# Kernel tuning notes

Measured on AMD Instinct MI355X. Metric: run time of the kernel, lower is better.

Reference implementation:

```python
import jax, jax.numpy as jnp
import numpy as np

NUM_EMBEDDINGS = 512
EMBEDDING_DIM = 128
COMMITMENT_COST = 0.25


def setup_inputs() -> dict:
    key = jax.random.key(0)
    k1, k2 = jax.random.split(key)
    inputs = jax.random.normal(k1, (8, EMBEDDING_DIM, 32, 32, 32), dtype=jnp.float32)
    limit = 1.0 / NUM_EMBEDDINGS
    weight = jax.random.uniform(k2, (NUM_EMBEDDINGS, EMBEDDING_DIM), dtype=jnp.float32,
                                minval=-limit, maxval=limit)
    return {"inputs": inputs, "weight": weight}


def reference(inputs, weight):
    sg = jax.lax.stop_gradient
    # (B, C, D, H, W) -> (B, D, H, W, C)
    x = jnp.transpose(inputs, (0, 2, 3, 4, 1))
    C = x.shape[-1]
    flat = x.reshape(-1, C)  # [N, C]
    distances = (jnp.sum(flat * flat, axis=1, keepdims=True)
                 + jnp.sum(weight * weight, axis=1)
                 - 2.0 * flat @ weight.T)
    encoding_indices = jnp.argmin(distances, axis=1)  # [N]
    encodings = jax.nn.one_hot(encoding_indices, weight.shape[0], dtype=jnp.float32)  # [N, E]
    # gather is mathematically identical to encodings @ weight
    quantized = weight[encoding_indices].reshape(x.shape)
    e_latent_loss = jnp.mean((sg(quantized) - x) ** 2)
    q_latent_loss = jnp.mean((quantized - sg(x)) ** 2)
    loss = q_latent_loss + COMMITMENT_COST * e_latent_loss
    # straight-through estimator
    quantized_st = x + sg(quantized - x)
    avg_probs = jnp.mean(encodings, axis=0)
    perplexity = jnp.exp(-jnp.sum(avg_probs * jnp.log(avg_probs + 1e-10)))
    out_q = jnp.transpose(quantized_st, (0, 4, 1, 2, 3))  # back to (B, C, D, H, W)
    return loss, out_q, perplexity, encodings
```

## Files before the change

kernel.cpp:

```cpp
#include <hip/hip_runtime.h>
#include <math.h>

#define CDIM 128
#define EDIM 512
#define BLK 256
#define MT 64
#define NVEC 262144
#define SPATIAL 32768
#define QELEMS 33554432LL
#define TIE_T 4e-6f

typedef __bf16 bf16x8 __attribute__((ext_vector_type(8)));
typedef float  f32x4  __attribute__((ext_vector_type(4)));

struct WS {
  float  wnh[EDIM];
  int    counts[EDIM];
  double lossAcc;
  double _pad;
  unsigned short wph[EDIM * CDIM];
  unsigned short wpl[EDIM * CDIM];
};

__device__ inline unsigned short bfbits(float f) {
  union { __bf16 b; unsigned short u; } cv; cv.b = (__bf16)f; return cv.u;
}
__device__ inline void split2(float x0, float x1, unsigned& hv, unsigned& lv) {
  unsigned short h0 = bfbits(x0), h1 = bfbits(x1);
  float r0 = x0 - __uint_as_float((unsigned)h0 << 16);
  float r1 = x1 - __uint_as_float((unsigned)h1 << 16);
  unsigned short l0 = bfbits(r0), l1 = bfbits(r1);
  hv = (unsigned)h0 | ((unsigned)h1 << 16);
  lv = (unsigned)l0 | ((unsigned)l1 << 16);
}

__device__ inline void ins3(float v, int ix, float& m1, float& m2, float& m3,
                            int& j1, int& j2) {
  bool q1 = (v < m1) || (v == m1 && ix < j1);
  bool q2 = (v < m2) || (v == m2 && ix < j2);
  if (q1)      { m3 = m2; m2 = m1; j2 = j1; m1 = v; j1 = ix; }
  else if (q2) { m3 = m2; m2 = v; j2 = ix; }
  else if (v < m3) { m3 = v; }
}

__global__ __launch_bounds__(256) void vq_pre(const float* __restrict__ wt,
                                              WS* __restrict__ ws, int buildWP) {
  const int tid = threadIdx.x, bid = blockIdx.x;
  const int e = bid * 8 + (tid >> 5);
  const int k0 = (tid & 31) * 4;
  float4 F = *(const float4*)(wt + (size_t)e * CDIM + k0);
  float nrm = F.x * F.x + F.y * F.y + F.z * F.z + F.w * F.w;
#pragma unroll
  for (int off = 1; off < 32; off <<= 1) nrm += __shfl_xor(nrm, off);
  if ((tid & 31) == 0) ws->wnh[e] = 0.5f * nrm;
  if (tid < 8) ws->counts[bid * 8 + tid] = 0;
  if (bid == 0 && tid == 0) ws->lossAcc = 0.0;
  if (buildWP) {
    const int etile = e >> 4, row = e & 15;
    const int kt = k0 >> 5, g = (k0 >> 3) & 3, j0 = k0 & 7;
    size_t idx = ((size_t)(etile * 4 + kt) * 64 + g * 16 + row) * 8 + j0;
    unsigned hv0, lv0, hv1, lv1;
    split2(F.x, F.y, hv0, lv0);
    split2(F.z, F.w, hv1, lv1);
    *(uint2*)&ws->wph[idx] = make_uint2(hv0, hv1);
    *(uint2*)&ws->wpl[idx] = make_uint2(lv0, lv1);
  }
}

__device__ double score64(const float* __restrict__ in, const float* __restrict__ wt,
                          size_t xoff, int e) {
  const float* w = wt + (size_t)e * CDIM;
  double a = 0.0;
  for (int c = 0; c < CDIM; ++c) {
    double wd = (double)w[c];
    double xv = (double)in[xoff + (size_t)c * SPATIAL];
    a = fma(wd, fma(0.5, wd, -xv), a);
  }
  return a;
}

template <bool USEWP>
__global__ __launch_bounds__(BLK, 4) void vq_main(const float* __restrict__ in,
                                                  const float* __restrict__ wt,
                                                  WS* __restrict__ ws,
                                                  float* __restrict__ out_q,
                                                  float* __restrict__ enc) {
  __shared__ __align__(16) unsigned short xhi[8192];
  __shared__ __align__(16) unsigned short xlo[8192];
  __shared__ float cb1[MT][5], cb2[MT][5], cb3[MT][5];
  __shared__ int   ci1[MT][5], ci2[MT][5];
  __shared__ int    sIdx[MT];
  __shared__ double lredw[4];

  const int tid = threadIdx.x;
  const int n0 = blockIdx.x * MT;
  const int b  = n0 >> 15;
  const int s0 = n0 & (SPATIAL - 1);
  const size_t ibase = (size_t)b * CDIM * SPATIAL;

  {
    const int mq = tid & 15;
    const int cg = tid >> 4;
    const int m0 = mq * 4, c0 = cg * 8;
    float4 F[8];
#pragma unroll
    for (int i = 0; i < 8; ++i)
      F[i] = *(const float4*)(in + ibase + (size_t)(c0 + i) * SPATIAL + s0 + m0);
#pragma unroll
    for (int mi = 0; mi < 4; ++mi) {
      const int m = m0 + mi;
      unsigned hv[4], lv[4];
#pragma unroll
      for (int p = 0; p < 4; ++p)
        split2(((const float*)&F[2 * p])[mi], ((const float*)&F[2 * p + 1])[mi],
               hv[p], lv[p]);
      const int fm = (m & 15) ^ ((m & 15) >> 2);
      const int elem = cg * 512 + (m >> 4) * 128 + fm * 8;
      *(uint4*)&xhi[elem] = make_uint4(hv[0], hv[1], hv[2], hv[3]);
      *(uint4*)&xlo[elem] = make_uint4(lv[0], lv[1], lv[2], lv[3]);
    }
  }
  __syncthreads();

  const int lane = tid & 63, wv = tid >> 6;
  const int col = lane & 15, g = lane >> 4;
  const int fcol = col ^ (col >> 2);

  float b1[4], b2[4], b3[4]; int i1[4], i2[4];
#pragma unroll
  for (int i = 0; i < 4; ++i) { b1[i] = 1e30f; b2[i] = 1e30f; b3[i] = 1e30f; i1[i] = 0; i2[i] = 0; }

  for (int ch = 0; ch < 8; ++ch) {
    const int etile = ch * 4 + wv;
    bf16x8 ah[4], al[4];
    if (USEWP) {
#pragma unroll
      for (int kt = 0; kt < 4; ++kt) {
        size_t aoff = ((size_t)(etile * 4 + kt) * 64 + lane) * 8;
        ah[kt] = *(const bf16x8*)&ws->wph[aoff];
        al[kt] = *(const bf16x8*)&ws->wpl[aoff];
      }
    } else {
      const int e = etile * 16 + col;
#pragma unroll
      for (int kt = 0; kt < 4; ++kt) {
        const float* wp = wt + (size_t)e * CDIM + kt * 32 + g * 8;
        float4 Fa = *(const float4*)wp, Fb = *(const float4*)(wp + 4);
        float xf[8] = {Fa.x, Fa.y, Fa.z, Fa.w, Fb.x, Fb.y, Fb.z, Fb.w};
        bf16x8 h, l;
#pragma unroll
        for (int j = 0; j < 8; ++j) {
          __bf16 hb = (__bf16)xf[j];
          float r = xf[j] - (float)hb;
          h[j] = hb; l[j] = (__bf16)r;
        }
        ah[kt] = h; al[kt] = l;
      }
    }

    f32x4 acc[4];
#pragma unroll
    for (int mt = 0; mt < 4; ++mt) {
      f32x4 a = {0.f, 0.f, 0.f, 0.f};
#pragma unroll
      for (int kt = 0; kt < 4; ++kt) {
        const int xb = (kt * 4 + g) * 512 + mt * 128 + fcol * 8;
        bf16x8 bh = *(const bf16x8*)&xhi[xb];
        bf16x8 bl = *(const bf16x8*)&xlo[xb];
        a = __builtin_amdgcn_mfma_f32_16x16x32_bf16(ah[kt], bh, a, 0, 0, 0);
        a = __builtin_amdgcn_mfma_f32_16x16x32_bf16(ah[kt], bl, a, 0, 0, 0);
        a = __builtin_amdgcn_mfma_f32_16x16x32_bf16(al[kt], bh, a, 0, 0, 0);
      }
      acc[mt] = a;
    }

    const int e0 = ch * 64 + wv * 16 + g * 4;
    const float4 wn = *(const float4*)&ws->wnh[e0];
#pragma unroll
    for (int mt = 0; mt < 4; ++mt) {
#pragma unroll
      for (int r = 0; r < 4; ++r) {
        float sc = ((const float*)&wn)[r] - acc[mt][r];
        ins3(sc, e0 + r, b1[mt], b2[mt], b3[mt], i1[mt], i2[mt]);
      }
    }
  }

#pragma unroll
  for (int mt = 0; mt < 4; ++mt) {
#pragma unroll
    for (int sh = 0; sh < 2; ++sh) {
      const int off = 16 << sh;
      float p1 = __shfl_xor(b1[mt], off), p2 = __shfl_xor(b2[mt], off),
            p3 = __shfl_xor(b3[mt], off);
      int q1 = __shfl_xor(i1[mt], off), q2 = __shfl_xor(i2[mt], off);
      ins3(p1, q1, b1[mt], b2[mt], b3[mt], i1[mt], i2[mt]);
      ins3(p2, q2, b1[mt], b2[mt], b3[mt], i1[mt], i2[mt]);
      ins3(p3, 0x7fffffff, b1[mt], b2[mt], b3[mt], i1[mt], i2[mt]);
    }
  }
  if (g == 0) {
#pragma unroll
    for (int mt = 0; mt < 4; ++mt) {
      const int m = mt * 16 + col;
      cb1[m][wv] = b1[mt]; cb2[m][wv] = b2[mt]; cb3[m][wv] = b3[mt];
      ci1[m][wv] = i1[mt]; ci2[m][wv] = i2[mt];
    }
  }
  __syncthreads();

  if (tid < MT) {
    const int vec = tid;
    float m1 = cb1[vec][0], m2 = cb2[vec][0], m3 = cb3[vec][0];
    int j1 = ci1[vec][0], j2 = ci2[vec][0];
#pragma unroll
    for (int t = 1; t < 4; ++t) {
      ins3(cb1[vec][t], ci1[vec][t], m1, m2, m3, j1, j2);
      ins3(cb2[vec][t], ci2[vec][t], m1, m2, m3, j1, j2);
      ins3(cb3[vec][t], 0x7fffffff, m1, m2, m3, j1, j2);
    }
    int bi = j1;
    const size_t xoff = ibase + s0 + vec;
    if (m3 - m1 < TIE_T) {
      double bd = 1e300; int bj = 0;
      for (int e = 0; e < EDIM; ++e) {
        double a = score64(in, wt, xoff, e);
        if (a < bd) { bd = a; bj = e; }
      }
      bi = bj;
    } else if (m2 - m1 < TIE_T) {
      double s1 = score64(in, wt, xoff, j1);
      double s2 = score64(in, wt, xoff, j2);
      if (s2 < s1 || (s2 == s1 && j2 < j1)) bi = j2;
    }
    sIdx[vec] = bi;
    atomicAdd(&ws->counts[bi], 1);
  }
  __syncthreads();

  {
    const int vec = tid & (MT - 1);
    const int qd  = tid >> 6;
    const int bi  = sIdx[vec];
    const float* wq = wt + (size_t)bi * CDIM;
    const size_t gbase = ibase + s0 + vec;
    const int fv = (vec & 15) ^ ((vec & 15) >> 2);
    double ls = 0.0;
#pragma unroll
    for (int cc = 0; cc < 32; cc += 4) {
      const int c = qd * 32 + cc;
      const int elem = (c >> 3) * 512 + (vec >> 4) * 128 + fv * 8 + (c & 7);
      uint2 hq = *(const uint2*)&xhi[elem];
      uint2 lq = *(const uint2*)&xlo[elem];
      float xs0 = __uint_as_float(hq.x << 16)        + __uint_as_float(lq.x << 16);
      float xs1 = __uint_as_float(hq.x & 0xffff0000u) + __uint_as_float(lq.x & 0xffff0000u);
      float xs2 = __uint_as_float(hq.y << 16)        + __uint_as_float(lq.y << 16);
      float xs3 = __uint_as_float(hq.y & 0xffff0000u) + __uint_as_float(lq.y & 0xffff0000u);
      float4 qv = *(const float4*)(wq + c);
      __builtin_nontemporal_store(qv.x, out_q + gbase + (size_t)(c + 0) * SPATIAL);
      __builtin_nontemporal_store(qv.y, out_q + gbase + (size_t)(c + 1) * SPATIAL);
      __builtin_nontemporal_store(qv.z, out_q + gbase + (size_t)(c + 2) * SPATIAL);
      __builtin_nontemporal_store(qv.w, out_q + gbase + (size_t)(c + 3) * SPATIAL);
      double d0 = (double)qv.x - (double)xs0; ls = fma(d0, d0, ls);
      double d1 = (double)qv.y - (double)xs1; ls = fma(d1, d1, ls);
      double d2 = (double)qv.z - (double)xs2; ls = fma(d2, d2, ls);
      double d3 = (double)qv.w - (double)xs3; ls = fma(d3, d3, ls);
    }
#pragma unroll
    for (int off = 32; off > 0; off >>= 1) ls += __shfl_down(ls, off);
    if (lane == 0) lredw[wv] = ls;
  }
  __syncthreads();
  if (tid == 0) atomicAdd(&ws->lossAcc, lredw[0] + lredw[1] + lredw[2] + lredw[3]);

  {
    const size_t r0 = (size_t)blockIdx.x * MT;
    const int c0 = tid * 2;
    unsigned long long* e2 = (unsigned long long*)enc;
    for (int r = 0; r < MT; ++r) {
      int idx = sIdx[r];
      union { float2 f; unsigned long long u; } cvt;
      cvt.f.x = (idx == c0) ? 1.0f : 0.0f;
      cvt.f.y = (idx == c0 + 1) ? 1.0f : 0.0f;
      __builtin_nontemporal_store(cvt.u, e2 + (r0 + (size_t)r) * (EDIM / 2) + tid);
    }
  }
}

__global__ __launch_bounds__(512) void vq_fin(const WS* __restrict__ ws, float* __restrict__ out) {
  __shared__ double red[EDIM];
  int t = threadIdx.x;
  double p = (double)ws->counts[t] * (1.0 / (double)NVEC);
  red[t] = p * log(p + 1e-10);
  __syncthreads();
  for (int off = 256; off > 0; off >>= 1) {
    if (t < off) red[t] += red[t + off];
    __syncthreads();
  }
  if (t == 0) {
    out[0] = (float)(1.25 * ws->lossAcc / (double)QELEMS);
    out[1 + QELEMS] = (float)exp(-red[0]);
  }
}

extern "C" void kernel_launch(void* const* d_in, const int* in_sizes, int n_in,
                              void* d_out, int out_size, void* d_ws, size_t ws_size,
                              hipStream_t stream) {
  const float* in = (const float*)d_in[0];
  const float* wt = (const float*)d_in[1];
  float* out = (float*)d_out;
  WS* ws = (WS*)d_ws;

  float* out_q = out + 1;
  float* enc   = out + 2 + QELEMS;

  const bool useWP = (ws_size >= sizeof(WS));
  vq_pre<<<dim3(64), dim3(256), 0, stream>>>(wt, ws, useWP ? 1 : 0);
  if (useWP)
    vq_main<true><<<dim3(NVEC / MT), dim3(BLK), 0, stream>>>(in, wt, ws, out_q, enc);
  else
    vq_main<false><<<dim3(NVEC / MT), dim3(BLK), 0, stream>>>(in, wt, ws, out_q, enc);
  vq_fin<<<dim3(1), dim3(512), 0, stream>>>(ws, out);
}
```

Before: 1.275 ms.

## Stage codebook chunks through LDS with register double-buffering and block-local histogram

```diff
diff --git a/kernel.cpp b/kernel.cpp
--- a/kernel.cpp
+++ b/kernel.cpp
@@ -5,6 +5,9 @@
 #define EDIM 512
 #define BLK 256
 #define MT 64
+#define ECH 64
+#define NCH (EDIM / ECH)
+#define WROW 136
 #define NVEC 262144
 #define SPATIAL 32768
 #define QELEMS 33554432LL
@@ -56,14 +59,11 @@
   if (tid < 8) ws->counts[bid * 8 + tid] = 0;
   if (bid == 0 && tid == 0) ws->lossAcc = 0.0;
   if (buildWP) {
-    const int etile = e >> 4, row = e & 15;
-    const int kt = k0 >> 5, g = (k0 >> 3) & 3, j0 = k0 & 7;
-    size_t idx = ((size_t)(etile * 4 + kt) * 64 + g * 16 + row) * 8 + j0;
     unsigned hv0, lv0, hv1, lv1;
     split2(F.x, F.y, hv0, lv0);
     split2(F.z, F.w, hv1, lv1);
-    *(uint2*)&ws->wph[idx] = make_uint2(hv0, hv1);
-    *(uint2*)&ws->wpl[idx] = make_uint2(lv0, lv1);
+    *(uint2*)&ws->wph[(size_t)e * CDIM + k0] = make_uint2(hv0, hv1);
+    *(uint2*)&ws->wpl[(size_t)e * CDIM + k0] = make_uint2(lv0, lv1);
   }
 }
 
@@ -80,15 +80,15 @@
 }
 
 template <bool USEWP>
-__global__ __launch_bounds__(BLK, 4) void vq_main(const float* __restrict__ in,
+__global__ __launch_bounds__(BLK, 2) void vq_main(const float* __restrict__ in,
                                                   const float* __restrict__ wt,
                                                   WS* __restrict__ ws,
                                                   float* __restrict__ out_q,
                                                   float* __restrict__ enc) {
   __shared__ __align__(16) unsigned short xhi[8192];
   __shared__ __align__(16) unsigned short xlo[8192];
-  __shared__ float cb1[MT][5], cb2[MT][5], cb3[MT][5];
-  __shared__ int   ci1[MT][5], ci2[MT][5];
+  __shared__ __align__(16) unsigned short wls[2 * ECH * WROW];
+  __shared__ int    hist[EDIM];
   __shared__ int    sIdx[MT];
   __shared__ double lredw[4];
 
@@ -97,6 +97,8 @@
   const int b  = n0 >> 15;
   const int s0 = n0 & (SPATIAL - 1);
   const size_t ibase = (size_t)b * CDIM * SPATIAL;
+
+  for (int e = tid; e < EDIM; e += BLK) hist[e] = 0;
 
   {
     const int mq = tid & 15;
@@ -120,42 +122,64 @@
       *(uint4*)&xlo[elem] = make_uint4(lv[0], lv[1], lv[2], lv[3]);
     }
   }
-  __syncthreads();
 
   const int lane = tid & 63, wv = tid >> 6;
   const int col = lane & 15, g = lane >> 4;
   const int fcol = col ^ (col >> 2);
 
+  const int se  = tid >> 2;
+  const int skq = (tid & 3) * 32;
+
   float b1[4], b2[4], b3[4]; int i1[4], i2[4];
 #pragma unroll
   for (int i = 0; i < 4; ++i) { b1[i] = 1e30f; b2[i] = 1e30f; b3[i] = 1e30f; i1[i] = 0; i2[i] = 0; }
 
-  for (int ch = 0; ch < 8; ++ch) {
-    const int etile = ch * 4 + wv;
+  uint4 Gh[4], Gl[4], Hh[4], Hl[4];
+#pragma unroll
+  for (int i = 0; i < 4; ++i) {
+    Hh[i] = make_uint4(0, 0, 0, 0);
+    Hl[i] = make_uint4(0, 0, 0, 0);
+  }
+
+  auto loadW = [&](int ch, uint4* Th, uint4* Tl) {
+    if (USEWP) {
+      const uint4* ph = (const uint4*)&ws->wph[(size_t)(ch * ECH + se) * CDIM + skq];
+      const uint4* pl = (const uint4*)&ws->wpl[(size_t)(ch * ECH + se) * CDIM + skq];
+#pragma unroll
+      for (int i = 0; i < 4; ++i) { Th[i] = ph[i]; Tl[i] = pl[i]; }
+    } else {
+      const float* wp = wt + (size_t)(ch * ECH + se) * CDIM + skq;
+#pragma unroll
+      for (int i = 0; i < 4; ++i) {
+        float4 A = *(const float4*)(wp + i * 8);
+        float4 B = *(const float4*)(wp + i * 8 + 4);
+        unsigned hv0, lv0, hv1, lv1, hv2, lv2, hv3, lv3;
+        split2(A.x, A.y, hv0, lv0); split2(A.z, A.w, hv1, lv1);
+        split2(B.x, B.y, hv2, lv2); split2(B.z, B.w, hv3, lv3);
+        Th[i] = make_uint4(hv0, hv1, hv2, hv3);
+        Tl[i] = make_uint4(lv0, lv1, lv2, lv3);
+      }
+    }
+  };
+
+  loadW(0, Gh, Gl);
+
+  for (int ch = 0; ch < NCH; ++ch) {
+    __syncthreads();
+#pragma unroll
+    for (int i = 0; i < 4; ++i) {
+      *(uint4*)&wls[se * WROW + skq + i * 8] = Gh[i];
+      *(uint4*)&wls[ECH * WROW + se * WROW + skq + i * 8] = Gl[i];
+    }
+    if (ch + 1 < NCH) loadW(ch + 1, Hh, Hl);
+    __syncthreads();
+
     bf16x8 ah[4], al[4];
-    if (USEWP) {
-#pragma unroll
-      for (int kt = 0; kt < 4; ++kt) {
-        size_t aoff = ((size_t)(etile * 4 + kt) * 64 + lane) * 8;
-        ah[kt] = *(const bf16x8*)&ws->wph[aoff];
-        al[kt] = *(const bf16x8*)&ws->wpl[aoff];
-      }
-    } else {
-      const int e = etile * 16 + col;
-#pragma unroll
-      for (int kt = 0; kt < 4; ++kt) {
-        const float* wp = wt + (size_t)e * CDIM + kt * 32 + g * 8;
-        float4 Fa = *(const float4*)wp, Fb = *(const float4*)(wp + 4);
-        float xf[8] = {Fa.x, Fa.y, Fa.z, Fa.w, Fb.x, Fb.y, Fb.z, Fb.w};
-        bf16x8 h, l;
-#pragma unroll
-        for (int j = 0; j < 8; ++j) {
-          __bf16 hb = (__bf16)xf[j];
-          float r = xf[j] - (float)hb;
-          h[j] = hb; l[j] = (__bf16)r;
-        }
-        ah[kt] = h; al[kt] = l;
-      }
+#pragma unroll
+    for (int kt = 0; kt < 4; ++kt) {
+      const int rb = (wv * 16 + col) * WROW + kt * 32 + g * 8;
+      ah[kt] = *(const bf16x8*)&wls[rb];
+      al[kt] = *(const bf16x8*)&wls[ECH * WROW + rb];
     }
 
     f32x4 acc[4];
@@ -174,7 +198,7 @@
       acc[mt] = a;
     }
 
-    const int e0 = ch * 64 + wv * 16 + g * 4;
+    const int e0 = ch * ECH + wv * 16 + g * 4;
     const float4 wn = *(const float4*)&ws->wnh[e0];
 #pragma unroll
     for (int mt = 0; mt < 4; ++mt) {
@@ -184,6 +208,8 @@
         ins3(sc, e0 + r, b1[mt], b2[mt], b3[mt], i1[mt], i2[mt]);
       }
     }
+#pragma unroll
+    for (int i = 0; i < 4; ++i) { Gh[i] = Hh[i]; Gl[i] = Hl[i]; }
   }
 
 #pragma unroll
@@ -199,42 +225,53 @@
       ins3(p3, 0x7fffffff, b1[mt], b2[mt], b3[mt], i1[mt], i2[mt]);
     }
   }
-  if (g == 0) {
-#pragma unroll
-    for (int mt = 0; mt < 4; ++mt) {
-      const int m = mt * 16 + col;
-      cb1[m][wv] = b1[mt]; cb2[m][wv] = b2[mt]; cb3[m][wv] = b3[mt];
-      ci1[m][wv] = i1[mt]; ci2[m][wv] = i2[mt];
-    }
-  }
+
   __syncthreads();
-
-  if (tid < MT) {
-    const int vec = tid;
-    float m1 = cb1[vec][0], m2 = cb2[vec][0], m3 = cb3[vec][0];
-    int j1 = ci1[vec][0], j2 = ci2[vec][0];
-#pragma unroll
-    for (int t = 1; t < 4; ++t) {
-      ins3(cb1[vec][t], ci1[vec][t], m1, m2, m3, j1, j2);
-      ins3(cb2[vec][t], ci2[vec][t], m1, m2, m3, j1, j2);
-      ins3(cb3[vec][t], 0x7fffffff, m1, m2, m3, j1, j2);
-    }
-    int bi = j1;
-    const size_t xoff = ibase + s0 + vec;
-    if (m3 - m1 < TIE_T) {
-      double bd = 1e300; int bj = 0;
-      for (int e = 0; e < EDIM; ++e) {
-        double a = score64(in, wt, xoff, e);
-        if (a < bd) { bd = a; bj = e; }
-      }
-      bi = bj;
-    } else if (m2 - m1 < TIE_T) {
-      double s1 = score64(in, wt, xoff, j1);
-      double s2 = score64(in, wt, xoff, j2);
-      if (s2 < s1 || (s2 == s1 && j2 < j1)) bi = j2;
-    }
-    sIdx[vec] = bi;
-    atomicAdd(&ws->counts[bi], 1);
+  {
+    char* mb = (char*)wls;
+    float (*cb1)[5] = (float(*)[5])mb;
+    float (*cb2)[5] = (float(*)[5])(mb + 1280);
+    float (*cb3)[5] = (float(*)[5])(mb + 2560);
+    int   (*ci1)[5] = (int(*)[5])(mb + 3840);
+    int   (*ci2)[5] = (int(*)[5])(mb + 5120);
+
+    if (g == 0) {
+#pragma unroll
+      for (int mt = 0; mt < 4; ++mt) {
+        const int m = mt * 16 + col;
+        cb1[m][wv] = b1[mt]; cb2[m][wv] = b2[mt]; cb3[m][wv] = b3[mt];
+        ci1[m][wv] = i1[mt]; ci2[m][wv] = i2[mt];
+      }
+    }
+    __syncthreads();
+
+    if (tid < MT) {
+      const int vec = tid;
+      float m1 = cb1[vec][0], m2 = cb2[vec][0], m3 = cb3[vec][0];
+      int j1 = ci1[vec][0], j2 = ci2[vec][0];
+#pragma unroll
+      for (int t = 1; t < 4; ++t) {
+        ins3(cb1[vec][t], ci1[vec][t], m1, m2, m3, j1, j2);
+        ins3(cb2[vec][t], ci2[vec][t], m1, m2, m3, j1, j2);
+        ins3(cb3[vec][t], 0x7fffffff, m1, m2, m3, j1, j2);
+      }
+      int bi = j1;
+      const size_t xoff = ibase + s0 + vec;
+      if (m3 - m1 < TIE_T) {
+        double bd = 1e300; int bj = 0;
+        for (int e = 0; e < EDIM; ++e) {
+          double a = score64(in, wt, xoff, e);
+          if (a < bd) { bd = a; bj = e; }
+        }
+        bi = bj;
+      } else if (m2 - m1 < TIE_T) {
+        double s1 = score64(in, wt, xoff, j1);
+        double s2 = score64(in, wt, xoff, j2);
+        if (s2 < s1 || (s2 == s1 && j2 < j1)) bi = j2;
+      }
+      sIdx[vec] = bi;
+      atomicAdd(&hist[bi], 1);
+    }
   }
   __syncthreads();
 
@@ -285,6 +322,11 @@
       __builtin_nontemporal_store(cvt.u, e2 + (r0 + (size_t)r) * (EDIM / 2) + tid);
     }
   }
+
+  for (int e = tid; e < EDIM; e += BLK) {
+    int v = hist[e];
+    if (v) atomicAdd(&ws->counts[e], v);
+  }
 }
 
 __global__ __launch_bounds__(512) void vq_fin(const WS* __restrict__ ws, float* __restrict__ out) {
```

Result: faster. 1.058 ms (-17.1%).

## Switch to fp16 split-x MFMA with LDS-staged codebook and wave-level tie resolution

Applied to the files above, without the earlier changes.

```diff
diff --git a/kernel.cpp b/kernel.cpp
--- a/kernel.cpp
+++ b/kernel.cpp
@@ -5,13 +5,15 @@
 #define EDIM 512
 #define BLK 256
 #define MT 64
+#define ECH 64
+#define NCH 8
 #define NVEC 262144
 #define SPATIAL 32768
 #define QELEMS 33554432LL
-#define TIE_T 4e-6f
-
-typedef __bf16 bf16x8 __attribute__((ext_vector_type(8)));
-typedef float  f32x4  __attribute__((ext_vector_type(4)));
+#define TIE_T 2.5e-4f
+
+typedef _Float16 f16x8 __attribute__((ext_vector_type(8)));
+typedef float    f32x4 __attribute__((ext_vector_type(4)));
 
 struct WS {
   float  wnh[EDIM];
@@ -19,20 +21,7 @@
   double lossAcc;
   double _pad;
   unsigned short wph[EDIM * CDIM];
-  unsigned short wpl[EDIM * CDIM];
 };
-
-__device__ inline unsigned short bfbits(float f) {
-  union { __bf16 b; unsigned short u; } cv; cv.b = (__bf16)f; return cv.u;
-}
-__device__ inline void split2(float x0, float x1, unsigned& hv, unsigned& lv) {
-  unsigned short h0 = bfbits(x0), h1 = bfbits(x1);
-  float r0 = x0 - __uint_as_float((unsigned)h0 << 16);
-  float r1 = x1 - __uint_as_float((unsigned)h1 << 16);
-  unsigned short l0 = bfbits(r0), l1 = bfbits(r1);
-  hv = (unsigned)h0 | ((unsigned)h1 << 16);
-  lv = (unsigned)l0 | ((unsigned)l1 << 16);
-}
 
 __device__ inline void ins3(float v, int ix, float& m1, float& m2, float& m3,
                             int& j1, int& j2) {
@@ -56,27 +45,14 @@
   if (tid < 8) ws->counts[bid * 8 + tid] = 0;
   if (bid == 0 && tid == 0) ws->lossAcc = 0.0;
   if (buildWP) {
-    const int etile = e >> 4, row = e & 15;
-    const int kt = k0 >> 5, g = (k0 >> 3) & 3, j0 = k0 & 7;
-    size_t idx = ((size_t)(etile * 4 + kt) * 64 + g * 16 + row) * 8 + j0;
-    unsigned hv0, lv0, hv1, lv1;
-    split2(F.x, F.y, hv0, lv0);
-    split2(F.z, F.w, hv1, lv1);
-    *(uint2*)&ws->wph[idx] = make_uint2(hv0, hv1);
-    *(uint2*)&ws->wpl[idx] = make_uint2(lv0, lv1);
-  }
-}
-
-__device__ double score64(const float* __restrict__ in, const float* __restrict__ wt,
-                          size_t xoff, int e) {
-  const float* w = wt + (size_t)e * CDIM;
-  double a = 0.0;
-  for (int c = 0; c < CDIM; ++c) {
-    double wd = (double)w[c];
-    double xv = (double)in[xoff + (size_t)c * SPATIAL];
-    a = fma(wd, fma(0.5, wd, -xv), a);
-  }
-  return a;
+    union { _Float16 h[4]; uint2 u; } P;
+    P.h[0] = (_Float16)F.x; P.h[1] = (_Float16)F.y;
+    P.h[2] = (_Float16)F.z; P.h[3] = (_Float16)F.w;
+    size_t idx = (size_t)(e >> 6) * 8192 +
+                 (size_t)(((((e >> 4) & 3) * 4 + (k0 >> 5)) * 64) +
+                          ((k0 >> 3) & 3) * 16 + (e & 15)) * 8 + (k0 & 7);
+    *(uint2*)&ws->wph[idx] = P.u;
+  }
 }
 
 template <bool USEWP>
@@ -85,190 +61,214 @@
                                                   WS* __restrict__ ws,
                                                   float* __restrict__ out_q,
                                                   float* __restrict__ enc) {
-  __shared__ __align__(16) unsigned short xhi[8192];
-  __shared__ __align__(16) unsigned short xlo[8192];
-  __shared__ float cb1[MT][5], cb2[MT][5], cb3[MT][5];
-  __shared__ int   ci1[MT][5], ci2[MT][5];
+  __shared__ __align__(16) char uni[32768];
+  __shared__ int    hist[EDIM];
   __shared__ int    sIdx[MT];
   __shared__ double lredw[4];
 
   const int tid = threadIdx.x;
+  const int lane = tid & 63, wv = tid >> 6;
+  const int col = lane & 15, g = lane >> 4;
+  const int fcol = col ^ (col >> 2);
   const int n0 = blockIdx.x * MT;
   const int b  = n0 >> 15;
   const int s0 = n0 & (SPATIAL - 1);
   const size_t ibase = (size_t)b * CDIM * SPATIAL;
 
-  {
-    const int mq = tid & 15;
-    const int cg = tid >> 4;
+  for (int e = tid; e < EDIM; e += BLK) hist[e] = 0;
+
+  uint4 G[4];
+  auto loadG = [&](int ch) {
+    if (USEWP) {
+      const uint4* p = (const uint4*)ws->wph + (size_t)ch * 1024;
+#pragma unroll
+      for (int i = 0; i < 4; ++i) G[i] = p[i * BLK + tid];
+    } else {
+#pragma unroll
+      for (int i = 0; i < 4; ++i) {
+        int q = i * BLK + tid;
+        int e = ch * 64 + (q >> 8) * 16 + (q & 15);
+        int kb = ((q >> 6) & 3) * 32 + ((q >> 4) & 3) * 8;
+        float4 A = *(const float4*)(wt + (size_t)e * CDIM + kb);
+        float4 Bv = *(const float4*)(wt + (size_t)e * CDIM + kb + 4);
+        union { _Float16 h[8]; uint4 u; } P;
+        P.h[0]=(_Float16)A.x; P.h[1]=(_Float16)A.y; P.h[2]=(_Float16)A.z; P.h[3]=(_Float16)A.w;
+        P.h[4]=(_Float16)Bv.x; P.h[5]=(_Float16)Bv.y; P.h[6]=(_Float16)Bv.z; P.h[7]=(_Float16)Bv.w;
+        G[i] = P.u;
+      }
+    }
+  };
+
+  {
+    const int mq = tid & 15, cg = tid >> 4;
     const int m0 = mq * 4, c0 = cg * 8;
     float4 F[8];
 #pragma unroll
     for (int i = 0; i < 8; ++i)
       F[i] = *(const float4*)(in + ibase + (size_t)(c0 + i) * SPATIAL + s0 + m0);
+    loadG(0);
+    _Float16* xh = (_Float16*)uni;
+    _Float16* xl = (_Float16*)(uni + 16384);
 #pragma unroll
     for (int mi = 0; mi < 4; ++mi) {
       const int m = m0 + mi;
-      unsigned hv[4], lv[4];
-#pragma unroll
-      for (int p = 0; p < 4; ++p)
-        split2(((const float*)&F[2 * p])[mi], ((const float*)&F[2 * p + 1])[mi],
-               hv[p], lv[p]);
+      union { _Float16 h[8]; uint4 u; } H, L;
+#pragma unroll
+      for (int p = 0; p < 8; ++p) {
+        float f = ((const float*)&F[p])[mi];
+        _Float16 hh = (_Float16)f;
+        H.h[p] = hh;
+        L.h[p] = (_Float16)(f - (float)hh);
+      }
       const int fm = (m & 15) ^ ((m & 15) >> 2);
       const int elem = cg * 512 + (m >> 4) * 128 + fm * 8;
-      *(uint4*)&xhi[elem] = make_uint4(hv[0], hv[1], hv[2], hv[3]);
-      *(uint4*)&xlo[elem] = make_uint4(lv[0], lv[1], lv[2], lv[3]);
+      *(uint4*)&xh[elem] = H.u;
+      *(uint4*)&xl[elem] = L.u;
     }
   }
   __syncthreads();
 
-  const int lane = tid & 63, wv = tid >> 6;
-  const int col = lane & 15, g = lane >> 4;
-  const int fcol = col ^ (col >> 2);
-
-  float b1[4], b2[4], b3[4]; int i1[4], i2[4];
-#pragma unroll
-  for (int i = 0; i < 4; ++i) { b1[i] = 1e30f; b2[i] = 1e30f; b3[i] = 1e30f; i1[i] = 0; i2[i] = 0; }
-
-  for (int ch = 0; ch < 8; ++ch) {
-    const int etile = ch * 4 + wv;
-    bf16x8 ah[4], al[4];
-    if (USEWP) {
+  f16x8 bh[4], bl[4];
+  {
+    const _Float16* xh = (const _Float16*)uni;
+    const _Float16* xl = (const _Float16*)(uni + 16384);
+#pragma unroll
+    for (int kt = 0; kt < 4; ++kt) {
+      const int eo = (kt * 4 + g) * 512 + wv * 128 + fcol * 8;
+      bh[kt] = *(const f16x8*)(xh + eo);
+      bl[kt] = *(const f16x8*)(xl + eo);
+    }
+  }
+
+  float b1 = 1e30f, b2 = 1e30f, b3 = 1e30f;
+  int i1v = 0, i2v = 0;
+
+  for (int ch = 0; ch < NCH; ++ch) {
+    __syncthreads();
+#pragma unroll
+    for (int i = 0; i < 4; ++i)
+      *(uint4*)(uni + (size_t)(i * BLK + tid) * 16) = G[i];
+    if (ch + 1 < NCH) loadG(ch + 1);
+    asm volatile("s_waitcnt lgkmcnt(0)" ::: "memory");
+    __builtin_amdgcn_sched_barrier(0);
+    __builtin_amdgcn_s_barrier();
+
+    const _Float16* wb = (const _Float16*)uni;
+#pragma unroll
+    for (int et = 0; et < 4; ++et) {
+      f16x8 ah[4];
+#pragma unroll
+      for (int kt = 0; kt < 4; ++kt)
+        ah[kt] = *(const f16x8*)(wb + ((et * 4 + kt) * 64 + lane) * 8);
+      f32x4 a = {0.f, 0.f, 0.f, 0.f};
 #pragma unroll
       for (int kt = 0; kt < 4; ++kt) {
-        size_t aoff = ((size_t)(etile * 4 + kt) * 64 + lane) * 8;
-        ah[kt] = *(const bf16x8*)&ws->wph[aoff];
-        al[kt] = *(const bf16x8*)&ws->wpl[aoff];
-      }
-    } else {
-      const int e = etile * 16 + col;
-#pragma unroll
-      for (int kt = 0; kt < 4; ++kt) {
-        const float* wp = wt + (size_t)e * CDIM + kt * 32 + g * 8;
-        float4 Fa = *(const float4*)wp, Fb = *(const float4*)(wp + 4);
-        float xf[8] = {Fa.x, Fa.y, Fa.z, Fa.w, Fb.x, Fb.y, Fb.z, Fb.w};
-        bf16x8 h, l;
-#pragma unroll
-        for (int j = 0; j < 8; ++j) {
-          __bf16 hb = (__bf16)xf[j];
-          float r = xf[j] - (float)hb;
-          h[j] = hb; l[j] = (__bf16)r;
+        a = __builtin_amdgcn_mfma_f32_16x16x32_f16(ah[kt], bh[kt], a, 0, 0, 0);
+        a = __builtin_amdgcn_mfma_f32_16x16x32_f16(ah[kt], bl[kt], a, 0, 0, 0);
+      }
+      const int e0 = ch * ECH + et * 16 + g * 4;
+      const float4 wn = *(const float4*)(ws->wnh + e0);
+#pragma unroll
+      for (int r = 0; r < 4; ++r) {
+        float sc = ((const float*)&wn)[r] - a[r];
+        ins3(sc, e0 + r, b1, b2, b3, i1v, i2v);
+      }
+    }
+  }
+
+#pragma unroll
+  for (int sh = 0; sh < 2; ++sh) {
+    const int off = 16 << sh;
+    float p1 = __shfl_xor(b1, off), p2 = __shfl_xor(b2, off), p3 = __shfl_xor(b3, off);
+    int q1 = __shfl_xor(i1v, off), q2 = __shfl_xor(i2v, off);
+    ins3(p1, q1, b1, b2, b3, i1v, i2v);
+    ins3(p2, q2, b1, b2, b3, i1v, i2v);
+    ins3(p3, 0x7fffffff, b1, b2, b3, i1v, i2v);
+  }
+
+  {
+    const bool t2 = (b2 - b1 < TIE_T);
+    const bool t3 = (b3 - b1 < TIE_T);
+    if (g == 0 && !t2 && !t3) { sIdx[wv * 16 + col] = i1v; atomicAdd(&hist[i1v], 1); }
+    unsigned long long mask = __ballot(t2 || t3) & 0xFFFFull;
+    float* scr = (float*)(uni + 16384 + wv * 512);
+    while (mask) {
+      const int bsel = __ffsll((unsigned long long)mask) - 1;
+      mask &= mask - 1;
+      if (col == bsel) {
+#pragma unroll
+        for (int kt = 0; kt < 4; ++kt)
+#pragma unroll
+          for (int j = 0; j < 8; ++j)
+            scr[kt * 32 + g * 8 + j] = (float)bh[kt][j] + (float)bl[kt][j];
+      }
+      asm volatile("s_waitcnt lgkmcnt(0)" ::: "memory");
+      __builtin_amdgcn_sched_barrier(0);
+      const int j1s = __shfl(i1v, bsel), j2s = __shfl(i2v, bsel);
+      const int isfull = __shfl((int)t3, bsel);
+      int bi;
+      if (isfull) {
+        double bd = 1e300; int bj = 0x7fffffff;
+        for (int i = 0; i < 8; ++i) {
+          const int e = lane * 8 + i;
+          const float* w = wt + (size_t)e * CDIM;
+          double s = 0.0;
+#pragma unroll 4
+          for (int c = 0; c < CDIM; ++c) {
+            double wd = (double)w[c];
+            s = fma(wd, fma(0.5, wd, -(double)scr[c]), s);
+          }
+          if (s < bd || (s == bd && e < bj)) { bd = s; bj = e; }
         }
-        ah[kt] = h; al[kt] = l;
-      }
-    }
-
-    f32x4 acc[4];
-#pragma unroll
-    for (int mt = 0; mt < 4; ++mt) {
-      f32x4 a = {0.f, 0.f, 0.f, 0.f};
-#pragma unroll
-      for (int kt = 0; kt < 4; ++kt) {
-        const int xb = (kt * 4 + g) * 512 + mt * 128 + fcol * 8;
-        bf16x8 bh = *(const bf16x8*)&xhi[xb];
-        bf16x8 bl = *(const bf16x8*)&xlo[xb];
-        a = __builtin_amdgcn_mfma_f32_16x16x32_bf16(ah[kt], bh, a, 0, 0, 0);
-        a = __builtin_amdgcn_mfma_f32_16x16x32_bf16(ah[kt], bl, a, 0, 0, 0);
-        a = __builtin_amdgcn_mfma_f32_16x16x32_bf16(al[kt], bh, a, 0, 0, 0);
-      }
-      acc[mt] = a;
-    }
-
-    const int e0 = ch * 64 + wv * 16 + g * 4;
-    const float4 wn = *(const float4*)&ws->wnh[e0];
-#pragma unroll
-    for (int mt = 0; mt < 4; ++mt) {
-#pragma unroll
-      for (int r = 0; r < 4; ++r) {
-        float sc = ((const float*)&wn)[r] - acc[mt][r];
-        ins3(sc, e0 + r, b1[mt], b2[mt], b3[mt], i1[mt], i2[mt]);
-      }
-    }
-  }
-
-#pragma unroll
-  for (int mt = 0; mt < 4; ++mt) {
-#pragma unroll
-    for (int sh = 0; sh < 2; ++sh) {
-      const int off = 16 << sh;
-      float p1 = __shfl_xor(b1[mt], off), p2 = __shfl_xor(b2[mt], off),
-            p3 = __shfl_xor(b3[mt], off);
-      int q1 = __shfl_xor(i1[mt], off), q2 = __shfl_xor(i2[mt], off);
-      ins3(p1, q1, b1[mt], b2[mt], b3[mt], i1[mt], i2[mt]);
-      ins3(p2, q2, b1[mt], b2[mt], b3[mt], i1[mt], i2[mt]);
-      ins3(p3, 0x7fffffff, b1[mt], b2[mt], b3[mt], i1[mt], i2[mt]);
-    }
-  }
-  if (g == 0) {
-#pragma unroll
-    for (int mt = 0; mt < 4; ++mt) {
-      const int m = mt * 16 + col;
-      cb1[m][wv] = b1[mt]; cb2[m][wv] = b2[mt]; cb3[m][wv] = b3[mt];
-      ci1[m][wv] = i1[mt]; ci2[m][wv] = i2[mt];
+#pragma unroll
+        for (int off = 32; off > 0; off >>= 1) {
+          double od = __shfl_xor(bd, off); int oj = __shfl_xor(bj, off);
+          if (od < bd || (od == bd && oj < bj)) { bd = od; bj = oj; }
+        }
+        bi = bj;
+      } else {
+        const int cand = (lane < 32) ? j1s : j2s;
+        const int c0 = (lane & 31) * 4;
+        const float* w = wt + (size_t)cand * CDIM;
+        double p = 0.0;
+#pragma unroll
+        for (int cc = 0; cc < 4; ++cc) {
+          double wd = (double)w[c0 + cc];
+          p = fma(wd, fma(0.5, wd, -(double)scr[c0 + cc]), p);
+        }
+#pragma unroll
+        for (int off = 16; off > 0; off >>= 1) p += __shfl_xor(p, off);
+        double s1 = __shfl(p, 0), s2 = __shfl(p, 32);
+        bi = (s2 < s1 || (s2 == s1 && j2s < j1s)) ? j2s : j1s;
+      }
+      if (lane == 0) { sIdx[wv * 16 + bsel] = bi; atomicAdd(&hist[bi], 1); }
     }
   }
   __syncthreads();
 
-  if (tid < MT) {
-    const int vec = tid;
-    float m1 = cb1[vec][0], m2 = cb2[vec][0], m3 = cb3[vec][0];
-    int j1 = ci1[vec][0], j2 = ci2[vec][0];
-#pragma unroll
-    for (int t = 1; t < 4; ++t) {
-      ins3(cb1[vec][t], ci1[vec][t], m1, m2, m3, j1, j2);
-      ins3(cb2[vec][t], ci2[vec][t], m1, m2, m3, j1, j2);
-      ins3(cb3[vec][t], 0x7fffffff, m1, m2, m3, j1, j2);
-    }
-    int bi = j1;
-    const size_t xoff = ibase + s0 + vec;
-    if (m3 - m1 < TIE_T) {
-      double bd = 1e300; int bj = 0;
-      for (int e = 0; e < EDIM; ++e) {
-        double a = score64(in, wt, xoff, e);
-        if (a < bd) { bd = a; bj = e; }
-      }
-      bi = bj;
-    } else if (m2 - m1 < TIE_T) {
-      double s1 = score64(in, wt, xoff, j1);
-      double s2 = score64(in, wt, xoff, j2);
-      if (s2 < s1 || (s2 == s1 && j2 < j1)) bi = j2;
-    }
-    sIdx[vec] = bi;
-    atomicAdd(&ws->counts[bi], 1);
-  }
-  __syncthreads();
-
-  {
-    const int vec = tid & (MT - 1);
-    const int qd  = tid >> 6;
-    const int bi  = sIdx[vec];
+  {
+    const int m = wv * 16 + col;
+    const int bi = sIdx[m];
     const float* wq = wt + (size_t)bi * CDIM;
-    const size_t gbase = ibase + s0 + vec;
-    const int fv = (vec & 15) ^ ((vec & 15) >> 2);
-    double ls = 0.0;
-#pragma unroll
-    for (int cc = 0; cc < 32; cc += 4) {
-      const int c = qd * 32 + cc;
-      const int elem = (c >> 3) * 512 + (vec >> 4) * 128 + fv * 8 + (c & 7);
-      uint2 hq = *(const uint2*)&xhi[elem];
-      uint2 lq = *(const uint2*)&xlo[elem];
-      float xs0 = __uint_as_float(hq.x << 16)        + __uint_as_float(lq.x << 16);
-      float xs1 = __uint_as_float(hq.x & 0xffff0000u) + __uint_as_float(lq.x & 0xffff0000u);
-      float xs2 = __uint_as_float(hq.y << 16)        + __uint_as_float(lq.y << 16);
-      float xs3 = __uint_as_float(hq.y & 0xffff0000u) + __uint_as_float(lq.y & 0xffff0000u);
-      float4 qv = *(const float4*)(wq + c);
-      __builtin_nontemporal_store(qv.x, out_q + gbase + (size_t)(c + 0) * SPATIAL);
-      __builtin_nontemporal_store(qv.y, out_q + gbase + (size_t)(c + 1) * SPATIAL);
-      __builtin_nontemporal_store(qv.z, out_q + gbase + (size_t)(c + 2) * SPATIAL);
-      __builtin_nontemporal_store(qv.w, out_q + gbase + (size_t)(c + 3) * SPATIAL);
-      double d0 = (double)qv.x - (double)xs0; ls = fma(d0, d0, ls);
-      double d1 = (double)qv.y - (double)xs1; ls = fma(d1, d1, ls);
-      double d2 = (double)qv.z - (double)xs2; ls = fma(d2, d2, ls);
-      double d3 = (double)qv.w - (double)xs3; ls = fma(d3, d3, ls);
-    }
-#pragma unroll
-    for (int off = 32; off > 0; off >>= 1) ls += __shfl_down(ls, off);
-    if (lane == 0) lredw[wv] = ls;
+    const size_t gbase = ibase + s0 + m;
+    float ls = 0.f;
+#pragma unroll
+    for (int kt = 0; kt < 4; ++kt) {
+      const int cb = kt * 32 + g * 8;
+      float4 qa = *(const float4*)(wq + cb);
+      float4 qb = *(const float4*)(wq + cb + 4);
+      float qf[8] = {qa.x, qa.y, qa.z, qa.w, qb.x, qb.y, qb.z, qb.w};
+#pragma unroll
+      for (int j = 0; j < 8; ++j) {
+        float xs = (float)bh[kt][j] + (float)bl[kt][j];
+        float d = qf[j] - xs;
+        ls = fmaf(d, d, ls);
+        __builtin_nontemporal_store(qf[j], out_q + gbase + (size_t)(cb + j) * SPATIAL);
+      }
+    }
+#pragma unroll
+    for (int off = 32; off > 0; off >>= 1) ls += __shfl_xor(ls, off);
+    if (lane == 0) lredw[wv] = (double)ls;
   }
   __syncthreads();
   if (tid == 0) atomicAdd(&ws->lossAcc, lredw[0] + lredw[1] + lredw[2] + lredw[3]);
@@ -285,6 +285,11 @@
       __builtin_nontemporal_store(cvt.u, e2 + (r0 + (size_t)r) * (EDIM / 2) + tid);
     }
   }
+
+  for (int e = tid; e < EDIM; e += BLK) {
+    int v = hist[e];
+    if (v) atomicAdd(&ws->counts[e], v);
+  }
 }
 
 __global__ __launch_bounds__(512) void vq_fin(const WS* __restrict__ ws, float* __restrict__ out) {
```

New measurement: 1.071 ms. 1.19x faster.
